# Kernel optimization log

Hardware: AMD Instinct MI355X
Metric: run time of the kernel (lower is better)

## Reference

```python
import jax, jax.numpy as jnp
from jax import lax
import numpy as np
import math

B, T, D = 4, 4096, 1024
K, H = 128, 8
KH = K // H
KER = 4
M = 4 * D  # mlp hidden


def _ln(x, g, b):
    m = jnp.mean(x, axis=-1, keepdims=True)
    v = jnp.var(x, axis=-1, keepdims=True)
    return (x - m) / jnp.sqrt(v + 1e-5) * g + b


def setup_inputs() -> dict:
    key = jax.random.key(0)
    ks = jax.random.split(key, 20)
    s = lambda i, shape, sc=0.02: jax.random.normal(ks[i], shape, dtype=jnp.float32) * sc
    inp = {}
    inp["x"] = jax.random.normal(ks[0], (B, T, D), dtype=jnp.float32)
    inp["prev_eig"] = jax.random.normal(ks[1], (B, T, 2 * K), dtype=jnp.float32)
    inp["in_proj_w"] = s(2, (2 * K, D))
    inp["conv_w"] = s(3, (2 * K, 1, KER), 0.3)          # depthwise Conv1d weight
    inp["conv_b"] = s(4, (2 * K,), 0.02)
    inp["mem_gate"] = jnp.float32(-3.0)
    inp["mem_proj_w"] = jnp.eye(2 * K, dtype=jnp.float32) + s(5, (2 * K, 2 * K), 0.02)
    # log_decay uniform in [center-1, center+0.5], center = -2 + 1.5*(1/5)
    center = -2.0 + 1.5 * (1.0 / 5.0)
    inp["log_decay"] = jax.random.uniform(ks[6], (K,), dtype=jnp.float32, minval=center - 1.0, maxval=center + 0.5)
    inp["frequency"] = jnp.linspace(0.0, 2.0 * math.pi * (1.0 - 1.0 / K), K, dtype=jnp.float32)
    inp["coupling"] = jnp.eye(KH, dtype=jnp.float32)[None] + 0.01 * jax.random.normal(ks[7], (H, KH, KH), dtype=jnp.float32) / math.sqrt(KH)
    inp["out_proj_w"] = s(8, (D, 2 * K))
    inp["gate_w"] = s(9, (D, D))
    inp["gate_b"] = jnp.full((D,), -2.0, dtype=jnp.float32)
    inp["mlp_w1"] = s(10, (M, D))
    inp["mlp_b1"] = jnp.zeros((M,), jnp.float32)
    inp["mlp_w2"] = s(11, (D, M))
    inp["mlp_b2"] = jnp.zeros((D,), jnp.float32)
    inp["n1_g"] = jnp.ones((D,), jnp.float32)
    inp["n1_b"] = jnp.zeros((D,), jnp.float32)
    inp["n2_g"] = jnp.ones((D,), jnp.float32)
    inp["n2_b"] = jnp.zeros((D,), jnp.float32)
    return inp


def reference(x, prev_eig, in_proj_w, conv_w, conv_b, mem_gate, mem_proj_w,
              log_decay, frequency, coupling, out_proj_w, gate_w, gate_b,
              mlp_w1, mlp_b1, mlp_w2, mlp_b2, n1_g, n1_b, n2_g, n2_b):
    Bn, Tn, Dn = x.shape
    xn = _ln(x, n1_g, n1_b)
    beta = xn @ in_proj_w.T                                   # [B,T,2K]
    # depthwise causal conv: torch pad=ker-1 both sides then [:, :, :T] == left-pad ker-1 + valid
    ker = conv_w.shape[-1]
    bp = jnp.pad(beta, ((0, 0), (ker - 1, 0), (0, 0))).transpose(0, 2, 1)  # [B,2K,T+ker-1]
    beta = lax.conv_general_dilated(bp, conv_w, (1,), 'VALID',
                                    feature_group_count=conv_w.shape[0],
                                    dimension_numbers=('NCH', 'OIH', 'NCH'))
    beta = jax.nn.silu(beta.transpose(0, 2, 1) + conv_b)       # [B,T,2K]
    br, bi = jnp.split(beta, 2, axis=-1)                       # [B,T,K] each
    # memory injection (has_memory: layer_idx > 0)
    mg = jax.nn.sigmoid(mem_gate)
    pr, pi = jnp.split(prev_eig @ mem_proj_w.T, 2, axis=-1)
    br = br + mg * pr
    bi = bi + mg * pi
    # eigenstate evolution via zero-padded complex FFT convolution
    mag = jax.nn.sigmoid(log_decay)                            # [K]
    n = jnp.arange(Tn, dtype=x.dtype)
    mag_pow = mag[None, :] ** n[:, None]                       # [T,K]
    phase = n[:, None] * frequency[None, :]
    kern = mag_pow * (jnp.cos(phase) + 1j * jnp.sin(phase))    # complex [T,K]
    beta_c = br + 1j * bi
    Bf = jnp.fft.fft(jnp.pad(beta_c, ((0, 0), (0, Tn), (0, 0))), axis=1)  # [B,2T,K]
    Kf = jnp.fft.fft(jnp.pad(kern, ((0, Tn), (0, 0))), axis=0)            # [2T,K]
    c = jnp.fft.ifft(Bf * Kf[None], axis=1)[:, :Tn]
    cr, ci = c.real.astype(x.dtype), c.imag.astype(x.dtype)
    # per-head coupling, batched over heads
    Hh, Kh = coupling.shape[0], coupling.shape[1]
    cr = jnp.einsum('hjk,bthk->bthj', coupling, cr.reshape(Bn, Tn, Hh, Kh)).reshape(Bn, Tn, Hh * Kh)
    ci = jnp.einsum('hjk,bthk->bthj', coupling, ci.reshape(Bn, Tn, Hh, Kh)).reshape(Bn, Tn, Hh * Kh)
    eig = jnp.concatenate([cr, ci], axis=-1)                   # [B,T,2K]
    h = jax.nn.sigmoid(xn @ gate_w.T + gate_b) * (eig @ out_proj_w.T)
    x1 = x + h
    y = _ln(x1, n2_g, n2_b)
    x2 = x1 + jax.nn.silu(y @ mlp_w1.T + mlp_b1) @ mlp_w2.T + mlp_b2
    return (x2, eig)
```

## Files before the change

kernel.cpp:

```cpp
#include <hip/hip_runtime.h>
#include <hip/hip_bf16.h>
#include <math.h>

#define Bn 4
#define Tn 4096
#define Dn 1024
#define Kn 128
#define TWOK 256
#define Hn 8
#define Mmlp 4096
#define NROW (Bn * Tn)
#define TAPS 16

typedef __attribute__((ext_vector_type(8))) short bf16x8;
typedef __attribute__((ext_vector_type(4))) float floatx4;

__device__ __forceinline__ float sigmoidf_(float x) { return 1.f / (1.f + expf(-x)); }

__global__ __launch_bounds__(256) void f2bf_kernel(const float* __restrict__ in,
                                                   __hip_bfloat16* __restrict__ out,
                                                   int n) {
    const int i = (blockIdx.x * 256 + threadIdx.x) * 4;
    if (i >= n) return;
    const float4 v = *(const float4*)(in + i);
    out[i + 0] = __float2bfloat16(v.x);
    out[i + 1] = __float2bfloat16(v.y);
    out[i + 2] = __float2bfloat16(v.z);
    out[i + 3] = __float2bfloat16(v.w);
}

__global__ __launch_bounds__(256) void ln_kernel(const float* __restrict__ x,
                                                 const float* __restrict__ g,
                                                 const float* __restrict__ b,
                                                 __hip_bfloat16* __restrict__ out) {
    const int row = blockIdx.x;
    const float4* xr = (const float4*)(x + (size_t)row * Dn);
    float4 v = xr[threadIdx.x];
    float s = v.x + v.y + v.z + v.w;
    float ss = v.x * v.x + v.y * v.y + v.z * v.z + v.w * v.w;
    for (int off = 32; off; off >>= 1) {
        s += __shfl_down(s, off);
        ss += __shfl_down(ss, off);
    }
    __shared__ float rs[4], rss[4];
    const int wv = threadIdx.x >> 6, ln = threadIdx.x & 63;
    if (ln == 0) { rs[wv] = s; rss[wv] = ss; }
    __syncthreads();
    s = rs[0] + rs[1] + rs[2] + rs[3];
    ss = rss[0] + rss[1] + rss[2] + rss[3];
    const float mean = s * (1.f / Dn);
    const float var = ss * (1.f / Dn) - mean * mean;
    const float inv = rsqrtf(var + 1e-5f);
    const float4 gg = ((const float4*)g)[threadIdx.x];
    const float4 bb = ((const float4*)b)[threadIdx.x];
    __hip_bfloat16* op = out + (size_t)row * Dn + threadIdx.x * 4;
    op[0] = __float2bfloat16((v.x - mean) * inv * gg.x + bb.x);
    op[1] = __float2bfloat16((v.y - mean) * inv * gg.y + bb.y);
    op[2] = __float2bfloat16((v.z - mean) * inv * gg.z + bb.z);
    op[3] = __float2bfloat16((v.w - mean) * inv * gg.w + bb.w);
}

template <int EPI, typename CT>
__global__ __launch_bounds__(256, EPI == 5 ? 2 : 4)
void gemm_bf(const ushort* __restrict__ A,
             const ushort* __restrict__ B,
             CT* __restrict__ C,
             int M, int N, int Kd,
             const float* __restrict__ bias,
             const float* __restrict__ aux1,
             const __hip_bfloat16* __restrict__ aux2,
             const ushort* __restrict__ A2, const ushort* __restrict__ B2, int Kd2) {
    __shared__ ushort As[128 * 32];
    __shared__ ushort Bs[128 * 32];
    const int tid = threadIdx.x;
    const int nbx = gridDim.x;
    const int nblk = nbx * gridDim.y;
    int bid = blockIdx.y * nbx + blockIdx.x;
    if ((nblk & 7) == 0)
        bid = (bid & 7) * (nblk >> 3) + (bid >> 3);
    const int m0 = (bid / nbx) * 128, n0 = (bid % nbx) * 128;
    const int wave = tid >> 6, lane = tid & 63;
    const int wm = wave >> 1, wn = wave & 1;
    const int mlane = lane & 15, quad = lane >> 4;

    floatx4 acc[4][4] = {};

    {
        const ushort* Ap = A + (size_t)m0 * Kd;
        const ushort* Bp = B + (size_t)n0 * Kd;
        for (int k0 = 0; k0 < Kd; k0 += 32) {
#pragma unroll
            for (int q = 0; q < 2; ++q) {
                const int c = q * 256 + tid;
                const int row = c >> 2, kc = (c & 3) * 8;
                __builtin_amdgcn_global_load_lds(
                    (const __attribute__((address_space(1))) void*)(Ap + (size_t)row * Kd + k0 + kc),
                    (__attribute__((address_space(3))) void*)(As + c * 8), 16, 0, 0);
                __builtin_amdgcn_global_load_lds(
                    (const __attribute__((address_space(1))) void*)(Bp + (size_t)row * Kd + k0 + kc),
                    (__attribute__((address_space(3))) void*)(Bs + c * 8), 16, 0, 0);
            }
            __syncthreads();
            bf16x8 af[4], bfr[4];
#pragma unroll
            for (int t = 0; t < 4; ++t) {
                af[t]  = *(const bf16x8*)&As[(wm * 64 + t * 16 + mlane) * 32 + quad * 8];
                bfr[t] = *(const bf16x8*)&Bs[(wn * 64 + t * 16 + mlane) * 32 + quad * 8];
            }
#pragma unroll
            for (int i = 0; i < 4; ++i)
#pragma unroll
                for (int j = 0; j < 4; ++j)
                    acc[i][j] = __builtin_amdgcn_mfma_f32_16x16x32_bf16(af[i], bfr[j], acc[i][j], 0, 0, 0);
            __syncthreads();
        }
    }

    floatx4 acc2[EPI == 5 ? 4 : 1][EPI == 5 ? 4 : 1] = {};
    if constexpr (EPI == 5) {
        const ushort* Ap = A2 + (size_t)m0 * Kd2;
        const ushort* Bp = B2 + (size_t)n0 * Kd2;
        for (int k0 = 0; k0 < Kd2; k0 += 32) {
#pragma unroll
            for (int q = 0; q < 2; ++q) {
                const int c = q * 256 + tid;
                const int row = c >> 2, kc = (c & 3) * 8;
                __builtin_amdgcn_global_load_lds(
                    (const __attribute__((address_space(1))) void*)(Ap + (size_t)row * Kd2 + k0 + kc),
                    (__attribute__((address_space(3))) void*)(As + c * 8), 16, 0, 0);
                __builtin_amdgcn_global_load_lds(
                    (const __attribute__((address_space(1))) void*)(Bp + (size_t)row * Kd2 + k0 + kc),
                    (__attribute__((address_space(3))) void*)(Bs + c * 8), 16, 0, 0);
            }
            __syncthreads();
            bf16x8 af[4], bfr[4];
#pragma unroll
            for (int t = 0; t < 4; ++t) {
                af[t]  = *(const bf16x8*)&As[(wm * 64 + t * 16 + mlane) * 32 + quad * 8];
                bfr[t] = *(const bf16x8*)&Bs[(wn * 64 + t * 16 + mlane) * 32 + quad * 8];
            }
#pragma unroll
            for (int i = 0; i < 4; ++i)
#pragma unroll
                for (int j = 0; j < 4; ++j)
                    acc2[i][j] = __builtin_amdgcn_mfma_f32_16x16x32_bf16(af[i], bfr[j], acc2[i][j], 0, 0, 0);
            __syncthreads();
        }
    }

    float s_pre = 0.f;
    if constexpr (EPI == 1) s_pre = sigmoidf_(bias[0]);

    const int cbase = n0 + wn * 64 + mlane;
#pragma unroll
    for (int i = 0; i < 4; ++i) {
#pragma unroll
        for (int r = 0; r < 4; ++r) {
            const int row = m0 + wm * 64 + i * 16 + quad * 4 + r;
            const size_t ro = (size_t)row * N;
#pragma unroll
            for (int j = 0; j < 4; ++j) {
                const int col = cbase + j * 16;
                const float a = acc[i][j][r];
                float o;
                if constexpr (EPI == 0) {
                    o = a;
                } else if constexpr (EPI == 1) {
                    o = s_pre * a;
                } else if constexpr (EPI == 2) {
                    o = aux1[ro + col] + sigmoidf_(a + bias[col]) * __bfloat162float(aux2[ro + col]);
                } else if constexpr (EPI == 3) {
                    const float t = a + bias[col];
                    o = t * sigmoidf_(t);
                } else if constexpr (EPI == 4) {
                    o = a + bias[col] + aux1[ro + col];
                } else {
                    o = aux1[ro + col] + sigmoidf_(a + bias[col]) * acc2[i][j][r];
                }
                if constexpr (__is_same(CT, float)) C[ro + col] = o;
                else                                C[ro + col] = __float2bfloat16(o);
            }
        }
    }
}

#define TCH 256
#define BROWS (TCH + TAPS + 2)
#define UROWS (TCH + TAPS - 1)

__global__ __launch_bounds__(256) void cfc_kernel(const float* __restrict__ beta,
                                                  const float* __restrict__ mgp,
                                                  const float* __restrict__ conv_w,
                                                  const float* __restrict__ conv_b,
                                                  const float* __restrict__ log_decay,
                                                  const float* __restrict__ freq,
                                                  const float* __restrict__ coup,
                                                  float* __restrict__ eig,
                                                  __hip_bfloat16* __restrict__ eig_bf) {
    const int b = blockIdx.z, h = blockIdx.y, t0 = blockIdx.x * TCH;
    const int tid = threadIdx.x;

    __shared__ float sbeta[BROWS * 32];
    __shared__ float su[UROWS * 33];
    __shared__ float str[16 * TAPS], sti[16 * TAPS];
    __shared__ float scoup[16 * 16];
    __shared__ float scw[32 * 4], scb[32];

    auto chan = [&](int cg) { return (cg < 16) ? (h * 16 + cg) : (128 + h * 16 + cg - 16); };

    for (int idx = tid; idx < BROWS * 32; idx += 256) {
        const int r = idx >> 5, cg = idx & 31;
        const int t = t0 - (TAPS + 2) + r;
        sbeta[idx] = (t >= 0) ? beta[((size_t)b * Tn + t) * TWOK + chan(cg)] : 0.f;
    }
    for (int idx = tid; idx < UROWS * 32; idx += 256) {
        const int r = idx >> 5, cg = idx & 31;
        const int t = t0 - (TAPS - 1) + r;
        su[r * 33 + cg] = (t >= 0) ? mgp[((size_t)b * Tn + t) * TWOK + chan(cg)] : 0.f;
    }
    if (tid < 128) scw[tid] = conv_w[chan(tid >> 2) * 4 + (tid & 3)];
    else if (tid < 160) scb[tid - 128] = conv_b[chan(tid - 128)];
    scoup[tid] = coup[h * 256 + tid];
    {
        const int k = tid >> 4, d = tid & (TAPS - 1);
        const float mag = sigmoidf_(log_decay[h * 16 + k]);
        const float f = freq[h * 16 + k];
        const float p = powf(mag, (float)d);
        str[k * TAPS + d] = p * cosf(d * f);
        sti[k * TAPS + d] = p * sinf(d * f);
    }
    __syncthreads();

    for (int idx = tid; idx < UROWS * 32; idx += 256) {
        const int r = idx >> 5, cg = idx & 31;
        const int rb = r + 3;
        float v = sbeta[(rb - 3) * 32 + cg] * scw[cg * 4 + 0] +
                  sbeta[(rb - 2) * 32 + cg] * scw[cg * 4 + 1] +
                  sbeta[(rb - 1) * 32 + cg] * scw[cg * 4 + 2] +
                  sbeta[(rb - 0) * 32 + cg] * scw[cg * 4 + 3] + scb[cg];
        v = v * sigmoidf_(v);
        su[r * 33 + cg] += v;
    }
    __syncthreads();

    const int ru = tid + (TAPS - 1);
    float orr[16], oii[16];
#pragma unroll
    for (int j = 0; j < 16; ++j) { orr[j] = 0.f; oii[j] = 0.f; }
#pragma unroll 4
    for (int k = 0; k < 16; ++k) {
        float accr = 0.f, acci = 0.f;
#pragma unroll
        for (int d = 0; d < TAPS; ++d) {
            const float ur = su[(ru - d) * 33 + k];
            const float ui = su[(ru - d) * 33 + 16 + k];
            const float lr = str[k * TAPS + d], li = sti[k * TAPS + d];
            accr += lr * ur - li * ui;
            acci += lr * ui + li * ur;
        }
#pragma unroll
        for (int j = 0; j < 16; ++j) {
            orr[j] += scoup[j * 16 + k] * accr;
            oii[j] += scoup[j * 16 + k] * acci;
        }
    }
    const size_t base = ((size_t)b * Tn + t0 + tid) * TWOK + h * 16;
    float4* er = (float4*)(eig + base);
    float4* ei = (float4*)(eig + base + Kn);
#pragma unroll
    for (int q = 0; q < 4; ++q) {
        er[q] = make_float4(orr[4 * q], orr[4 * q + 1], orr[4 * q + 2], orr[4 * q + 3]);
        ei[q] = make_float4(oii[4 * q], oii[4 * q + 1], oii[4 * q + 2], oii[4 * q + 3]);
    }
#pragma unroll
    for (int j = 0; j < 16; ++j) {
        eig_bf[base + j] = __float2bfloat16(orr[j]);
        eig_bf[base + Kn + j] = __float2bfloat16(oii[j]);
    }
}

extern "C" void kernel_launch(void* const* d_in, const int* in_sizes, int n_in,
                              void* d_out, int out_size, void* d_ws, size_t ws_size,
                              hipStream_t stream) {
    const float* x          = (const float*)d_in[0];
    const float* prev_eig   = (const float*)d_in[1];
    const float* in_proj_w  = (const float*)d_in[2];
    const float* conv_w     = (const float*)d_in[3];
    const float* conv_b     = (const float*)d_in[4];
    const float* mem_gate   = (const float*)d_in[5];
    const float* mem_proj_w = (const float*)d_in[6];
    const float* log_decay  = (const float*)d_in[7];
    const float* frequency  = (const float*)d_in[8];
    const float* coupling   = (const float*)d_in[9];
    const float* out_proj_w = (const float*)d_in[10];
    const float* gate_w     = (const float*)d_in[11];
    const float* gate_b     = (const float*)d_in[12];
    const float* mlp_w1     = (const float*)d_in[13];
    const float* mlp_b1     = (const float*)d_in[14];
    const float* mlp_w2     = (const float*)d_in[15];
    const float* mlp_b2     = (const float*)d_in[16];
    const float* n1_g       = (const float*)d_in[17];
    const float* n1_b       = (const float*)d_in[18];
    const float* n2_g       = (const float*)d_in[19];
    const float* n2_b       = (const float*)d_in[20];

    float* out = (float*)d_out;
    float* eig = out + (size_t)NROW * Dn;

    char* wsb = (char*)d_ws;
    const size_t MB = 1 << 20;
    float* x1    = (float*)(wsb + 0);
    float* beta  = (float*)(wsb + 0);
    float* mgp   = (float*)(wsb + 16 * MB);
    __hip_bfloat16* h1      = (__hip_bfloat16*)(wsb + 64 * MB);
    __hip_bfloat16* eig_bf  = (__hip_bfloat16*)(wsb + 96 * MB);
    __hip_bfloat16* peig_bf = (__hip_bfloat16*)(wsb + 104 * MB);
    __hip_bfloat16* xn_bf   = (__hip_bfloat16*)(wsb + 128 * MB);
    __hip_bfloat16* y_bf    = (__hip_bfloat16*)(wsb + 160 * MB);
    __hip_bfloat16* w1_bf   = (__hip_bfloat16*)(wsb + 192 * MB);
    __hip_bfloat16* w2_bf   = (__hip_bfloat16*)(wsb + 200 * MB);
    __hip_bfloat16* gate_bf = (__hip_bfloat16*)(wsb + 208 * MB);
    __hip_bfloat16* inpj_bf = (__hip_bfloat16*)(wsb + 210 * MB);
    __hip_bfloat16* outpj_bf= (__hip_bfloat16*)(wsb + 210 * MB + 512 * 1024);
    __hip_bfloat16* mempj_bf= (__hip_bfloat16*)(wsb + 211 * MB);

    auto cvt = [&](const float* src, __hip_bfloat16* dst, int n) {
        f2bf_kernel<<<dim3((n / 4 + 255) / 256), dim3(256), 0, stream>>>(src, dst, n);
    };
    cvt(in_proj_w,  inpj_bf,  TWOK * Dn);
    cvt(mem_proj_w, mempj_bf, TWOK * TWOK);
    cvt(out_proj_w, outpj_bf, Dn * TWOK);
    cvt(gate_w,     gate_bf,  Dn * Dn);
    cvt(mlp_w1,     w1_bf,    Mmlp * Dn);
    cvt(mlp_w2,     w2_bf,    Dn * Mmlp);
    cvt(prev_eig,   peig_bf,  NROW * TWOK);

    ln_kernel<<<dim3(NROW), dim3(256), 0, stream>>>(x, n1_g, n1_b, xn_bf);
    gemm_bf<0, float><<<dim3(2, 128), dim3(256), 0, stream>>>(
        (const ushort*)xn_bf, (const ushort*)inpj_bf, beta, NROW, TWOK, Dn,
        nullptr, nullptr, nullptr, nullptr, nullptr, 0);
    gemm_bf<1, float><<<dim3(2, 128), dim3(256), 0, stream>>>(
        (const ushort*)peig_bf, (const ushort*)mempj_bf, mgp, NROW, TWOK, TWOK,
        mem_gate, nullptr, nullptr, nullptr, nullptr, 0);
    cfc_kernel<<<dim3(Tn / TCH, Hn, Bn), dim3(256), 0, stream>>>(
        beta, mgp, conv_w, conv_b, log_decay, frequency, coupling, eig, eig_bf);
    gemm_bf<5, float><<<dim3(8, 128), dim3(256), 0, stream>>>(
        (const ushort*)xn_bf, (const ushort*)gate_bf, x1, NROW, Dn, Dn,
        gate_b, x, nullptr, (const ushort*)eig_bf, (const ushort*)outpj_bf, TWOK);
    ln_kernel<<<dim3(NROW), dim3(256), 0, stream>>>(x1, n2_g, n2_b, y_bf);
    for (int ck = 0; ck < 2; ++ck) {
        const size_t roff = (size_t)ck * 8192 * Dn;
        gemm_bf<3, __hip_bfloat16><<<dim3(32, 64), dim3(256), 0, stream>>>(
            (const ushort*)(y_bf + roff), (const ushort*)w1_bf, h1, 8192, Mmlp, Dn,
            mlp_b1, nullptr, nullptr, nullptr, nullptr, 0);
        gemm_bf<4, float><<<dim3(8, 64), dim3(256), 0, stream>>>(
            (const ushort*)h1, (const ushort*)w2_bf, out + roff, 8192, Dn, Mmlp,
            mlp_b2, x1 + roff, nullptr, nullptr, nullptr, 0);
    }
}
```

Before: 793.5 us.

## Add 256x256-tile pipelined MFMA GEMM for MLP and unchunk when workspace allows

Adds a new 512-thread GEMM kernel with 256x256 output tiles and double-buffered direct global-to-LDS loads using an XOR swizzle. Its schedule interleaves MFMA groups with the next tile's loads, raises wave priority around the MFMAs, and remaps block IDs for L2 locality. Both MLP GEMMs now use this kernel. When the workspace is at least 252 MB, the buffers are relaid out so the MLP runs over all 16384 rows in one launch pair instead of two chunks. The aim is more reuse per tile and fewer launches, at the cost of higher register and LDS pressure and a tile count that may not fill every CU evenly.

```diff
diff --git a/kernel.cpp b/kernel.cpp
--- a/kernel.cpp
+++ b/kernel.cpp
@@ -176,6 +176,161 @@
                     o = a + bias[col] + aux1[ro + col];
                 } else {
                     o = aux1[ro + col] + sigmoidf_(a + bias[col]) * acc2[i][j][r];
+                }
+                if constexpr (__is_same(CT, float)) C[ro + col] = o;
+                else                                C[ro + col] = __float2bfloat16(o);
+            }
+        }
+    }
+}
+
+template <int EPI, typename CT>
+__global__ __launch_bounds__(512, 2)
+void gemm256(const ushort* __restrict__ A, const ushort* __restrict__ B,
+             CT* __restrict__ C, int N, int Kd,
+             const float* __restrict__ bias, const float* __restrict__ aux1,
+             const __hip_bfloat16* __restrict__ aux2) {
+    __shared__ ushort As[2][256 * 64];
+    __shared__ ushort Bs[2][256 * 64];
+    const int tid = threadIdx.x;
+    const int nbx = gridDim.x;
+    const int nblk = nbx * gridDim.y;
+    int bid = blockIdx.y * nbx + blockIdx.x;
+    if ((nblk & 7) == 0)
+        bid = (bid & 7) * (nblk >> 3) + (bid >> 3);
+    const int m0 = (bid / nbx) * 256, n0 = (bid % nbx) * 256;
+    const int wave = tid >> 6, lane = tid & 63;
+    const int wm = wave >> 2, wn = wave & 3;
+    const int mlane = lane & 15, quad = lane >> 4;
+    const int NT = Kd >> 6;
+
+    const int srow = tid >> 3;
+    const size_t sgoff = (size_t)srow * Kd + (size_t)(((tid & 7) ^ (srow & 7)) << 3);
+
+    auto stA = [&](int s, int half) {
+        const int r0 = half * 64;
+        const ushort* g = A + (size_t)(m0 + r0) * Kd + (s << 6) + sgoff;
+        ushort* l = &As[s & 1][(r0 << 6) + (tid << 3)];
+        __builtin_amdgcn_global_load_lds(
+            (const __attribute__((address_space(1))) void*)g,
+            (__attribute__((address_space(3))) void*)l, 16, 0, 0);
+        __builtin_amdgcn_global_load_lds(
+            (const __attribute__((address_space(1))) void*)(g + (size_t)128 * Kd),
+            (__attribute__((address_space(3))) void*)(l + (128 << 6)), 16, 0, 0);
+    };
+    auto stB = [&](int s, int half) {
+        const int r0 = half * 128;
+        const ushort* g = B + (size_t)(n0 + r0) * Kd + (s << 6) + sgoff;
+        ushort* l = &Bs[s & 1][(r0 << 6) + (tid << 3)];
+        __builtin_amdgcn_global_load_lds(
+            (const __attribute__((address_space(1))) void*)g,
+            (__attribute__((address_space(3))) void*)l, 16, 0, 0);
+        __builtin_amdgcn_global_load_lds(
+            (const __attribute__((address_space(1))) void*)(g + (size_t)64 * Kd),
+            (__attribute__((address_space(3))) void*)(l + (64 << 6)), 16, 0, 0);
+    };
+
+    floatx4 acc[8][4] = {};
+    bf16x8 a[4][2], b[4][2];
+
+    const int ar = (wm * 128 + mlane) << 6;
+    const int br = (wn * 64 + mlane) << 6;
+    const int o0 = (quad ^ (mlane & 7)) << 3;
+    const int o1 = ((4 + quad) ^ (mlane & 7)) << 3;
+
+#define MFMA16(MB, NB)                                                           \
+    __builtin_amdgcn_s_setprio(1);                                               \
+    _Pragma("unroll")                                                            \
+    for (int m_ = 0; m_ < 4; ++m_) {                                             \
+        _Pragma("unroll")                                                        \
+        for (int n_ = 0; n_ < 2; ++n_) {                                         \
+            acc[MB + m_][NB + n_] = __builtin_amdgcn_mfma_f32_16x16x32_bf16(     \
+                a[m_][0], b[NB + n_][0], acc[MB + m_][NB + n_], 0, 0, 0);        \
+            acc[MB + m_][NB + n_] = __builtin_amdgcn_mfma_f32_16x16x32_bf16(     \
+                a[m_][1], b[NB + n_][1], acc[MB + m_][NB + n_], 0, 0, 0);        \
+        }                                                                        \
+    }                                                                            \
+    __builtin_amdgcn_s_setprio(0);
+
+    stA(0, 0); stA(0, 1); stB(0, 0); stB(0, 1);
+    __builtin_amdgcn_sched_barrier(0);
+    stA(1, 0); stB(1, 0); stA(1, 1);
+    asm volatile("s_waitcnt vmcnt(6)" ::: "memory");
+    __builtin_amdgcn_s_barrier();
+
+    for (int t = 0; t < NT; ++t) {
+        const ushort* Ab = &As[t & 1][0];
+        const ushort* Bb = &Bs[t & 1][0];
+#pragma unroll
+        for (int m = 0; m < 4; ++m) {
+            a[m][0] = *(const bf16x8*)(Ab + ar + m * 1024 + o0);
+            a[m][1] = *(const bf16x8*)(Ab + ar + m * 1024 + o1);
+        }
+#pragma unroll
+        for (int n = 0; n < 2; ++n) {
+            b[n][0] = *(const bf16x8*)(Bb + br + n * 1024 + o0);
+            b[n][1] = *(const bf16x8*)(Bb + br + n * 1024 + o1);
+        }
+        if (t + 1 < NT) stB(t + 1, 1);
+        __builtin_amdgcn_s_barrier();
+        asm volatile("s_waitcnt lgkmcnt(0)" ::: "memory");
+        __builtin_amdgcn_sched_barrier(0);
+        MFMA16(0, 0)
+        __builtin_amdgcn_s_barrier();
+#pragma unroll
+        for (int n = 0; n < 2; ++n) {
+            b[2 + n][0] = *(const bf16x8*)(Bb + br + (2 + n) * 1024 + o0);
+            b[2 + n][1] = *(const bf16x8*)(Bb + br + (2 + n) * 1024 + o1);
+        }
+        if (t + 2 < NT) stA(t + 2, 0);
+        __builtin_amdgcn_s_barrier();
+        asm volatile("s_waitcnt lgkmcnt(0)" ::: "memory");
+        __builtin_amdgcn_sched_barrier(0);
+        MFMA16(0, 2)
+        __builtin_amdgcn_s_barrier();
+#pragma unroll
+        for (int m = 0; m < 4; ++m) {
+            a[m][0] = *(const bf16x8*)(Ab + ar + (4 + m) * 1024 + o0);
+            a[m][1] = *(const bf16x8*)(Ab + ar + (4 + m) * 1024 + o1);
+        }
+        if (t + 2 < NT) stB(t + 2, 0);
+        __builtin_amdgcn_s_barrier();
+        asm volatile("s_waitcnt lgkmcnt(0)" ::: "memory");
+        __builtin_amdgcn_sched_barrier(0);
+        MFMA16(4, 0)
+        __builtin_amdgcn_s_barrier();
+        if (t + 2 < NT) stA(t + 2, 1);
+        MFMA16(4, 2)
+        if (t + 2 < NT) {
+            asm volatile("s_waitcnt vmcnt(6)" ::: "memory");
+        } else if (t + 1 < NT) {
+            asm volatile("s_waitcnt vmcnt(0)" ::: "memory");
+        }
+        if (t + 1 < NT) __builtin_amdgcn_s_barrier();
+    }
+#undef MFMA16
+
+    const int cbase = n0 + wn * 64 + mlane;
+#pragma unroll
+    for (int m = 0; m < 8; ++m) {
+#pragma unroll
+        for (int r = 0; r < 4; ++r) {
+            const int row = m0 + wm * 128 + m * 16 + quad * 4 + r;
+            const size_t ro = (size_t)row * N;
+#pragma unroll
+            for (int n = 0; n < 4; ++n) {
+                const int col = cbase + n * 16;
+                const float av = acc[m][n][r];
+                float o;
+                if constexpr (EPI == 0) {
+                    o = av;
+                } else if constexpr (EPI == 2) {
+                    o = aux1[ro + col] + sigmoidf_(av + bias[col]) * __bfloat162float(aux2[ro + col]);
+                } else if constexpr (EPI == 3) {
+                    const float tt = av + bias[col];
+                    o = tt * sigmoidf_(tt);
+                } else {
+                    o = av + bias[col] + aux1[ro + col];
                 }
                 if constexpr (__is_same(CT, float)) C[ro + col] = o;
                 else                                C[ro + col] = __float2bfloat16(o);
@@ -309,20 +464,38 @@
 
     char* wsb = (char*)d_ws;
     const size_t MB = 1 << 20;
+    const bool bigws = ws_size >= 252 * MB;
+
     float* x1    = (float*)(wsb + 0);
     float* beta  = (float*)(wsb + 0);
     float* mgp   = (float*)(wsb + 16 * MB);
-    __hip_bfloat16* h1      = (__hip_bfloat16*)(wsb + 64 * MB);
-    __hip_bfloat16* eig_bf  = (__hip_bfloat16*)(wsb + 96 * MB);
-    __hip_bfloat16* peig_bf = (__hip_bfloat16*)(wsb + 104 * MB);
-    __hip_bfloat16* xn_bf   = (__hip_bfloat16*)(wsb + 128 * MB);
-    __hip_bfloat16* y_bf    = (__hip_bfloat16*)(wsb + 160 * MB);
-    __hip_bfloat16* w1_bf   = (__hip_bfloat16*)(wsb + 192 * MB);
-    __hip_bfloat16* w2_bf   = (__hip_bfloat16*)(wsb + 200 * MB);
-    __hip_bfloat16* gate_bf = (__hip_bfloat16*)(wsb + 208 * MB);
-    __hip_bfloat16* inpj_bf = (__hip_bfloat16*)(wsb + 210 * MB);
-    __hip_bfloat16* outpj_bf= (__hip_bfloat16*)(wsb + 210 * MB + 512 * 1024);
-    __hip_bfloat16* mempj_bf= (__hip_bfloat16*)(wsb + 211 * MB);
+    __hip_bfloat16 *h1, *eig_bf, *peig_bf, *xn_bf, *y_bf, *w1_bf, *w2_bf,
+                   *gate_bf, *inpj_bf, *outpj_bf, *mempj_bf;
+    if (bigws) {
+        h1       = (__hip_bfloat16*)(wsb + 64 * MB);
+        xn_bf    = (__hip_bfloat16*)(wsb + 192 * MB);
+        y_bf     = (__hip_bfloat16*)(wsb + 192 * MB);
+        w1_bf    = (__hip_bfloat16*)(wsb + 224 * MB);
+        w2_bf    = (__hip_bfloat16*)(wsb + 232 * MB);
+        gate_bf  = (__hip_bfloat16*)(wsb + 240 * MB);
+        inpj_bf  = (__hip_bfloat16*)(wsb + 242 * MB);
+        outpj_bf = (__hip_bfloat16*)(wsb + 242 * MB + 512 * 1024);
+        mempj_bf = (__hip_bfloat16*)(wsb + 243 * MB);
+        peig_bf  = (__hip_bfloat16*)(wsb + 244 * MB);
+        eig_bf   = (__hip_bfloat16*)(wsb + 244 * MB);
+    } else {
+        h1       = (__hip_bfloat16*)(wsb + 64 * MB);
+        eig_bf   = (__hip_bfloat16*)(wsb + 96 * MB);
+        peig_bf  = (__hip_bfloat16*)(wsb + 104 * MB);
+        xn_bf    = (__hip_bfloat16*)(wsb + 128 * MB);
+        y_bf     = (__hip_bfloat16*)(wsb + 160 * MB);
+        w1_bf    = (__hip_bfloat16*)(wsb + 192 * MB);
+        w2_bf    = (__hip_bfloat16*)(wsb + 200 * MB);
+        gate_bf  = (__hip_bfloat16*)(wsb + 208 * MB);
+        inpj_bf  = (__hip_bfloat16*)(wsb + 210 * MB);
+        outpj_bf = (__hip_bfloat16*)(wsb + 210 * MB + 512 * 1024);
+        mempj_bf = (__hip_bfloat16*)(wsb + 211 * MB);
+    }
 
     auto cvt = [&](const float* src, __hip_bfloat16* dst, int n) {
         f2bf_kernel<<<dim3((n / 4 + 255) / 256), dim3(256), 0, stream>>>(src, dst, n);
@@ -348,13 +521,22 @@
         (const ushort*)xn_bf, (const ushort*)gate_bf, x1, NROW, Dn, Dn,
         gate_b, x, nullptr, (const ushort*)eig_bf, (const ushort*)outpj_bf, TWOK);
     ln_kernel<<<dim3(NROW), dim3(256), 0, stream>>>(x1, n2_g, n2_b, y_bf);
-    for (int ck = 0; ck < 2; ++ck) {
-        const size_t roff = (size_t)ck * 8192 * Dn;
-        gemm_bf<3, __hip_bfloat16><<<dim3(32, 64), dim3(256), 0, stream>>>(
-            (const ushort*)(y_bf + roff), (const ushort*)w1_bf, h1, 8192, Mmlp, Dn,
-            mlp_b1, nullptr, nullptr, nullptr, nullptr, 0);
-        gemm_bf<4, float><<<dim3(8, 64), dim3(256), 0, stream>>>(
-            (const ushort*)h1, (const ushort*)w2_bf, out + roff, 8192, Dn, Mmlp,
-            mlp_b2, x1 + roff, nullptr, nullptr, nullptr, 0);
+    if (bigws) {
+        gemm256<3, __hip_bfloat16><<<dim3(16, 64), dim3(512), 0, stream>>>(
+            (const ushort*)y_bf, (const ushort*)w1_bf, h1, Mmlp, Dn,
+            mlp_b1, nullptr, nullptr);
+        gemm256<4, float><<<dim3(4, 64), dim3(512), 0, stream>>>(
+            (const ushort*)h1, (const ushort*)w2_bf, out, Dn, Mmlp,
+            mlp_b2, x1, nullptr);
+    } else {
+        for (int ck = 0; ck < 2; ++ck) {
+            const size_t roff = (size_t)ck * 8192 * Dn;
+            gemm256<3, __hip_bfloat16><<<dim3(16, 32), dim3(512), 0, stream>>>(
+                (const ushort*)(y_bf + roff), (const ushort*)w1_bf, h1, Mmlp, Dn,
+                mlp_b1, nullptr, nullptr);
+            gemm256<4, float><<<dim3(4, 32), dim3(512), 0, stream>>>(
+                (const ushort*)h1, (const ushort*)w2_bf, out + roff, Dn, Mmlp,
+                mlp_b2, x1 + roff, nullptr);
+        }
     }
 }
```

Result: faster. 723.5 us (-8.8%).
